# Kernel tuning notes

Hardware: AMD Instinct MI355X
Metric: run time of the kernel (lower is better)

The kernel has to match this reference:

```python
import jax, jax.numpy as jnp
import numpy as np

NUM_FEATURES = 50


def _build_port_feature_mask(num_node_features: int = NUM_FEATURES) -> np.ndarray:
    """(F, 6) mask: port p has track if any connect/port-revenue feature for p is nonzero."""
    mask = np.zeros((num_node_features, 6), dtype=np.float32)
    feat_idx = 23
    for i in range(6):
        for j in range(i):
            mask[feat_idx, i] = 1.0
            mask[feat_idx, j] = 1.0
            feat_idx += 1
    for i in range(6):
        for k in range(2):
            mask[38 + i * 2 + k, i] = 1.0
    return mask


def setup_inputs() -> dict:
    key = jax.random.key(0)
    k1, k2 = jax.random.split(key)
    B, N, F = 16, 1024, NUM_FEATURES
    node_features = jax.random.normal(k1, (B, N, F), dtype=jnp.float32)
    direction_matrix = jax.random.randint(k2, (N, N), 0, 7, dtype=jnp.int32)
    port_feature_mask = jnp.asarray(_build_port_feature_mask(F))
    return {
        "node_features": node_features,
        "direction_matrix": direction_matrix,
        "port_feature_mask": port_feature_mask,
    }


def reference(node_features, direction_matrix, port_feature_mask):
    B, N, _ = node_features.shape
    # (B, N, 6): per-hex, per-port track indicator
    port_activity = node_features @ port_feature_mask
    port_has_track = (port_activity > 0).astype(node_features.dtype)

    dir_mat = direction_matrix.astype(jnp.int32)
    adj_mask = (dir_mat != 6).astype(node_features.dtype)  # (N, N)
    dir_clamped = jnp.minimum(dir_mat, 5)                  # (N, N)
    opp_clamped = jnp.minimum((dir_mat + 3) % 6, 5)        # (N, N)

    i_idx = jnp.arange(N)[:, None]  # row index i, broadcasts with (N, N)
    j_idx = jnp.arange(N)[None, :]  # col index j
    # src[b, i, j] = port_has_track[b, i, dir_clamped[i, j]]
    src_ports = port_has_track[:, i_idx, dir_clamped]  # (B, N, N)
    # dst[b, i, j] = port_has_track[b, j, opp_clamped[i, j]]
    dst_ports = port_has_track[:, j_idx, opp_clamped]  # (B, N, N)

    return src_ports * dst_ports * adj_mask[None, :, :]
```

## Files before the change

### kernel.cpp

```cpp
#include <hip/hip_runtime.h>

#define N_NODES 1024
#define B_SZ 16
#define F_SZ 50

__global__ void ports_kernel(const float* __restrict__ nf,
                             const float* __restrict__ mask,
                             unsigned char* __restrict__ bits) {
    __shared__ float smask[F_SZ * 6];
    for (int t = threadIdx.x; t < F_SZ * 6; t += blockDim.x)
        smask[t] = mask[t];
    __syncthreads();

    int idx = blockIdx.x * blockDim.x + threadIdx.x;
    if (idx >= B_SZ * N_NODES) return;
    const float* row = nf + (size_t)idx * F_SZ;

    float acc[6] = {0.f, 0.f, 0.f, 0.f, 0.f, 0.f};
    for (int f = 0; f < F_SZ; ++f) {
        float v = row[f];
        #pragma unroll
        for (int p = 0; p < 6; ++p)
            acc[p] += v * smask[f * 6 + p];
    }
    unsigned char b = 0;
    #pragma unroll
    for (int p = 0; p < 6; ++p)
        if (acc[p] > 0.0f) b |= (unsigned char)(1u << p);
    bits[idx] = b;
}

__global__ void connect_kernel(const int* __restrict__ dir,
                               const unsigned char* __restrict__ bits,
                               float* __restrict__ out) {
    const int i = blockIdx.x;
    const int j4 = threadIdx.x;

    int4 d = ((const int4*)(dir + (size_t)i * N_NODES))[j4];
    int dv[4] = {d.x, d.y, d.z, d.w};
    unsigned ds[4], os[4], am[4];
    #pragma unroll
    for (int k = 0; k < 4; ++k) {
        am[k] = (dv[k] != 6) ? 1u : 0u;
        ds[k] = (unsigned)min(dv[k], 5);
        os[k] = (unsigned)min((dv[k] + 3) % 6, 5);
    }

    #pragma unroll
    for (int b = 0; b < B_SZ; ++b) {
        unsigned s = bits[b * N_NODES + i];
        uchar4 t = ((const uchar4*)(bits + b * N_NODES))[j4];
        unsigned tb[4] = {t.x, t.y, t.z, t.w};
        float4 o;
        float* op = (float*)&o;
        #pragma unroll
        for (int k = 0; k < 4; ++k)
            op[k] = ((s >> ds[k]) & (tb[k] >> os[k]) & am[k] & 1u) ? 1.0f : 0.0f;
        ((float4*)(out + (size_t)b * N_NODES * N_NODES + (size_t)i * N_NODES))[j4] = o;
    }
}

extern "C" void kernel_launch(void* const* d_in, const int* in_sizes, int n_in,
                              void* d_out, int out_size, void* d_ws, size_t ws_size,
                              hipStream_t stream) {
    const float* nf   = (const float*)d_in[0];
    const int*   dir  = (const int*)d_in[1];
    const float* mask = (const float*)d_in[2];
    float* out = (float*)d_out;
    unsigned char* bits = (unsigned char*)d_ws;

    ports_kernel<<<(B_SZ * N_NODES + 255) / 256, 256, 0, stream>>>(nf, mask, bits);
    connect_kernel<<<N_NODES, 256, 0, stream>>>(dir, bits, out);
}
```

Before: 24.03 us.

## Transpose port bits to node-major layout and vectorize loads in both kernels

The ports kernel now writes the per-port bitmask transposed (node-major, batch-minor), so the connect kernel can fetch all 16 batches for a node with one uint4 load instead of 16 separate byte loads. The ports kernel also uses 64-thread blocks with an unrolled float2 feature loop to raise block count and cut load instructions. The cost is byte-scattered, uncoalesced writes in the ports kernel and extra shift/mask work in the connect kernel, whose run time is dominated by the 64 MB output write.

New measurement: 24.84 us. 1.03x slower.

```diff
diff --git a/kernel.cpp b/kernel.cpp
--- a/kernel.cpp
+++ b/kernel.cpp
@@ -4,39 +4,46 @@
 #define B_SZ 16
 #define F_SZ 50
 
-__global__ void ports_kernel(const float* __restrict__ nf,
-                             const float* __restrict__ mask,
-                             unsigned char* __restrict__ bits) {
+__global__ __launch_bounds__(64) void ports_kernel(
+        const float* __restrict__ nf,
+        const float* __restrict__ mask,
+        unsigned char* __restrict__ bitsT) {
     __shared__ float smask[F_SZ * 6];
-    for (int t = threadIdx.x; t < F_SZ * 6; t += blockDim.x)
+    for (int t = threadIdx.x; t < F_SZ * 6; t += 64)
         smask[t] = mask[t];
     __syncthreads();
 
-    int idx = blockIdx.x * blockDim.x + threadIdx.x;
-    if (idx >= B_SZ * N_NODES) return;
-    const float* row = nf + (size_t)idx * F_SZ;
+    int idx = blockIdx.x * 64 + threadIdx.x;
+    int b = idx >> 10;
+    int n = idx & (N_NODES - 1);
+    const float2* row = (const float2*)(nf + (size_t)idx * F_SZ);
 
     float acc[6] = {0.f, 0.f, 0.f, 0.f, 0.f, 0.f};
-    for (int f = 0; f < F_SZ; ++f) {
-        float v = row[f];
+    #pragma unroll
+    for (int q = 0; q < F_SZ / 2; ++q) {
+        float2 v = row[q];
         #pragma unroll
         for (int p = 0; p < 6; ++p)
-            acc[p] += v * smask[f * 6 + p];
+            acc[p] += v.x * smask[(2 * q) * 6 + p];
+        #pragma unroll
+        for (int p = 0; p < 6; ++p)
+            acc[p] += v.y * smask[(2 * q + 1) * 6 + p];
     }
-    unsigned char b = 0;
+    unsigned char m = 0;
     #pragma unroll
     for (int p = 0; p < 6; ++p)
-        if (acc[p] > 0.0f) b |= (unsigned char)(1u << p);
-    bits[idx] = b;
+        if (acc[p] > 0.0f) m |= (unsigned char)(1u << p);
+    bitsT[n * B_SZ + b] = m;
 }
 
-__global__ void connect_kernel(const int* __restrict__ dir,
-                               const unsigned char* __restrict__ bits,
-                               float* __restrict__ out) {
+__global__ __launch_bounds__(256) void connect_kernel(
+        const int* __restrict__ dir,
+        const unsigned char* __restrict__ bitsT,
+        float* __restrict__ out) {
     const int i = blockIdx.x;
-    const int j4 = threadIdx.x;
+    const int t = threadIdx.x;
 
-    int4 d = ((const int4*)(dir + (size_t)i * N_NODES))[j4];
+    int4 d = ((const int4*)(dir + (size_t)i * N_NODES))[t];
     int dv[4] = {d.x, d.y, d.z, d.w};
     unsigned ds[4], os[4], am[4];
     #pragma unroll
@@ -46,17 +53,30 @@
         os[k] = (unsigned)min((dv[k] + 3) % 6, 5);
     }
 
+    const uint4* bt = (const uint4*)bitsT;
+    uint4 srcv = bt[i];
+    unsigned srcw[4] = {srcv.x, srcv.y, srcv.z, srcv.w};
+    uint4 dstv[4];
+    unsigned dstw[4][4];
+    #pragma unroll
+    for (int k = 0; k < 4; ++k) {
+        dstv[k] = bt[t * 4 + k];
+        dstw[k][0] = dstv[k].x; dstw[k][1] = dstv[k].y;
+        dstw[k][2] = dstv[k].z; dstw[k][3] = dstv[k].w;
+    }
+
+    float* obase = out + (size_t)i * N_NODES + (size_t)t * 4;
     #pragma unroll
     for (int b = 0; b < B_SZ; ++b) {
-        unsigned s = bits[b * N_NODES + i];
-        uchar4 t = ((const uchar4*)(bits + b * N_NODES))[j4];
-        unsigned tb[4] = {t.x, t.y, t.z, t.w};
+        unsigned s = (srcw[b >> 2] >> ((b & 3) * 8)) & 0x3fu;
         float4 o;
         float* op = (float*)&o;
         #pragma unroll
-        for (int k = 0; k < 4; ++k)
-            op[k] = ((s >> ds[k]) & (tb[k] >> os[k]) & am[k] & 1u) ? 1.0f : 0.0f;
-        ((float4*)(out + (size_t)b * N_NODES * N_NODES + (size_t)i * N_NODES))[j4] = o;
+        for (int k = 0; k < 4; ++k) {
+            unsigned tb = (dstw[k][b >> 2] >> ((b & 3) * 8)) & 0x3fu;
+            op[k] = ((s >> ds[k]) & (tb >> os[k]) & am[k] & 1u) ? 1.0f : 0.0f;
+        }
+        *(float4*)(obase + (size_t)b * N_NODES * N_NODES) = o;
     }
 }
 
@@ -67,8 +87,8 @@
     const int*   dir  = (const int*)d_in[1];
     const float* mask = (const float*)d_in[2];
     float* out = (float*)d_out;
-    unsigned char* bits = (unsigned char*)d_ws;
+    unsigned char* bitsT = (unsigned char*)d_ws;
 
-    ports_kernel<<<(B_SZ * N_NODES + 255) / 256, 256, 0, stream>>>(nf, mask, bits);
-    connect_kernel<<<N_NODES, 256, 0, stream>>>(dir, bits, out);
+    ports_kernel<<<(B_SZ * N_NODES) / 64, 64, 0, stream>>>(nf, mask, bitsT);
+    connect_kernel<<<N_NODES, 256, 0, stream>>>(dir, bitsT, out);
 }
```
